# Performance work log

Measured on AMD Instinct MI355X. Metric: run time of the kernel, lower is better.

## Reference

```python
import jax, jax.numpy as jnp
import numpy as np

D = 1024
H = 16
DH = D // H

def setup_inputs() -> dict:
    key = jax.random.key(0)
    k1, k2, k3, k4 = jax.random.split(key, 4)
    x = jax.random.normal(k1, (4, 2048, D), dtype=jnp.float32)
    # qkv_linear: Linear(D, D, bias=False); weight stored as (out, in) torch-style
    w_qkv = jax.random.normal(k2, (D, D), dtype=jnp.float32) * (1.0 / np.sqrt(D))
    # final linear: Linear(D, D) with bias
    w_out = jax.random.normal(k3, (D, D), dtype=jnp.float32) * (1.0 / np.sqrt(D))
    b_out = jax.random.normal(k4, (D,), dtype=jnp.float32) * 0.01
    return {"x": x, "w_qkv": w_qkv, "w_out": w_out, "b_out": b_out}

def reference(x, w_qkv, w_out, b_out):
    B, S, E = x.shape
    # Same projection used for Q, K, V (faithful to original module)
    qkv = jnp.einsum('bse,de->bsd', x, w_qkv)           # [B,S,D]
    qkv = qkv.reshape(B, S, H, DH).transpose(0, 2, 1, 3)  # [B,H,S,Dh]
    q = k = v = qkv
    scale = DH ** -0.5
    attn = jnp.einsum('bhqd,bhkd->bhqk', q, k) * scale   # [B,H,S,S]
    attn = jax.nn.softmax(attn, axis=-1)
    out = jnp.einsum('bhqk,bhkd->bhqd', attn, v)         # [B,H,S,Dh]
    out = out.transpose(0, 2, 1, 3).reshape(B, S, E)
    return jnp.einsum('bse,de->bsd', out, w_out) + b_out
```

## Files before the change

kernel.cpp:

```cpp
#include <hip/hip_runtime.h>
#include <hip/hip_bf16.h>
#include <stdint.h>

typedef unsigned short u16;
typedef unsigned int   u32;
typedef unsigned long long u64;
typedef __bf16 bf16x8 __attribute__((ext_vector_type(8)));
typedef float  f32x4  __attribute__((ext_vector_type(4)));

#define D_MODEL 1024
#define NH 16
#define DHEAD 64
#define BB 4
#define SS 2048
#define MM (BB*SS)

__device__ __forceinline__ u16 f2bf(float f) {
    unsigned int u = __float_as_uint(f);
    u += 0x7fffu + ((u >> 16) & 1u);
    return (u16)(u >> 16);
}
__device__ __forceinline__ float bf2f(u16 s) {
    return __uint_as_float(((unsigned int)s) << 16);
}
__device__ __forceinline__ u32 pkbf(float a, float b) {
    __hip_bfloat162 h = __float22bfloat162_rn(make_float2(a, b));
    return *(u32*)&h;
}

union U8 {
    uint4 q;
    u16   v[8];
    bf16x8 f;
};

#define N4X (MM * D_MODEL / 4)
#define N4W (D_MODEL * D_MODEL / 4)
__global__ __launch_bounds__(256) void cvt_all_kernel(const float* __restrict__ x,
                                                      const float* __restrict__ wq,
                                                      const float* __restrict__ wo,
                                                      u16* __restrict__ xb,
                                                      u16* __restrict__ wqb,
                                                      u16* __restrict__ wob) {
    int i = blockIdx.x * 256 + threadIdx.x;
    const float* s; u16* d; int off;
    if (i < N4X)            { s = x;  d = xb;  off = i; }
    else if (i < N4X + N4W) { s = wq; d = wqb; off = i - N4X; }
    else                    { s = wo; d = wob; off = i - N4X - N4W; }
    float4 f = ((const float4*)s)[off];
    u32 o[2] = { pkbf(f.x, f.y), pkbf(f.z, f.w) };
    ((uint2*)d)[off] = *(const uint2*)o;
}

template <bool PERMUTE_OUT>
__device__ __forceinline__ void gemm_body(const u16* __restrict__ A,
                                          const u16* __restrict__ Bt,
                                          const float* __restrict__ Bo,
                                          u16* __restrict__ Cq, u16* __restrict__ CqT,
                                          float* __restrict__ Out)
{
    __shared__ __align__(16) u16 As[128*64];
    __shared__ __align__(16) u16 Bs[128*64];

    const int tid  = threadIdx.x;
    const int wave = tid >> 6;
    const int lane = tid & 63;
    const int quad = lane >> 4;
    const int l16  = lane & 15;
    const int bm = blockIdx.x >> 3;
    const int bn = blockIdx.x & 7;
    const int wm = wave >> 1, wn = wave & 1;

    f32x4 acc[4][4] = {};

    const int rp = tid >> 3;
    const int ch = tid & 7;
    const int sc = ch ^ (rp & 7);

    const u16* Ab = A  + (size_t)(bm * 128 + rp) * D_MODEL + sc * 8;
    const u16* Bb = Bt + (size_t)(bn * 128 + rp) * D_MODEL + sc * 8;
    const int xr = l16 & 7;

    for (int k0 = 0; k0 < D_MODEL; k0 += 64) {
#pragma unroll
        for (int p = 0; p < 4; ++p) {
            __builtin_amdgcn_global_load_lds(
                (__attribute__((address_space(1))) void*)(Ab + (size_t)(32*p) * D_MODEL + k0),
                (__attribute__((address_space(3))) void*)(As + p*2048 + tid*8), 16, 0, 0);
            __builtin_amdgcn_global_load_lds(
                (__attribute__((address_space(1))) void*)(Bb + (size_t)(32*p) * D_MODEL + k0),
                (__attribute__((address_space(3))) void*)(Bs + p*2048 + tid*8), 16, 0, 0);
        }
        __syncthreads();

#pragma unroll
        for (int ks = 0; ks < 2; ++ks) {
            bf16x8 af[4], bfr[4];
#pragma unroll
            for (int t = 0; t < 4; ++t)
                af[t] = *(const bf16x8*)(const void*)(
                    As + (wm*64 + t*16 + l16)*64 + (((ks*4 + quad) ^ xr) * 8));
#pragma unroll
            for (int t = 0; t < 4; ++t)
                bfr[t] = *(const bf16x8*)(const void*)(
                    Bs + (wn*64 + t*16 + l16)*64 + (((ks*4 + quad) ^ xr) * 8));
#pragma unroll
            for (int i = 0; i < 4; ++i)
#pragma unroll
                for (int j = 0; j < 4; ++j)
                    acc[i][j] = __builtin_amdgcn_mfma_f32_16x16x32_bf16(af[i], bfr[j], acc[i][j], 0, 0, 0);
        }
        __syncthreads();
    }

    const int rowbase = bm*128 + wm*64;
    const int colbase = bn*128 + wn*64;
    if (PERMUTE_OUT) {
#pragma unroll
        for (int j = 0; j < 4; ++j) {
            const int col = colbase + j*16 + l16;
            const int h = col >> 6, dh = col & 63;
#pragma unroll
            for (int i = 0; i < 4; ++i) {
                const int row0 = rowbase + i*16 + quad*4;
                const int b = row0 >> 11, s0 = row0 & (SS - 1);
#pragma unroll
                for (int r = 0; r < 4; ++r)
                    Cq[(((size_t)(b*NH + h))*SS + s0 + r)*DHEAD + dh] = f2bf(acc[i][j][r]);
                u64 w = (u64)pkbf(acc[i][j][0], acc[i][j][1])
                      | ((u64)pkbf(acc[i][j][2], acc[i][j][3]) << 32);
                *(u64*)(CqT + ((size_t)((b*NH + h)*DHEAD + dh))*SS + s0) = w;
            }
        }
    } else {
#pragma unroll
        for (int j = 0; j < 4; ++j) {
            const int col = colbase + j*16 + l16;
            const float bias = Bo[col];
#pragma unroll
            for (int i = 0; i < 4; ++i) {
#pragma unroll
                for (int r = 0; r < 4; ++r) {
                    const int row = rowbase + i*16 + quad*4 + r;
                    Out[(size_t)row * D_MODEL + col] = acc[i][j][r] + bias;
                }
            }
        }
    }
}

__global__ __launch_bounds__(256) void gemm_qkv_kernel(const u16* __restrict__ A,
                                                       const u16* __restrict__ Bt,
                                                       u16* __restrict__ Cq,
                                                       u16* __restrict__ CqT) {
    gemm_body<true>(A, Bt, nullptr, Cq, CqT, nullptr);
}

__global__ __launch_bounds__(256) void gemm_out_kernel(const u16* __restrict__ A,
                                                       const u16* __restrict__ Bt,
                                                       const float* __restrict__ Bo,
                                                       float* __restrict__ Out) {
    gemm_body<false>(A, Bt, Bo, nullptr, nullptr, Out);
}

__global__ __launch_bounds__(256, 4) void attn_kernel(const u16* __restrict__ qkv,
                                                      const u16* __restrict__ qkvT,
                                                      u16* __restrict__ outb)
{
    __shared__ __align__(16) u16 Ks[2*2048];
    __shared__ __align__(16) u16 Vt[2*2048];
    __shared__ __align__(16) u16 Pl[4*1280];

    const int tid  = threadIdx.x;
    const int wave = tid >> 6;
    const int lane = tid & 63;
    const int quad = lane >> 4;
    const int l16  = lane & 15;

    const int bh   = blockIdx.x >> 4;
    const int qblk = blockIdx.x & 15;
    const int b = bh >> 4, h = bh & 15;
    const int qbase = qblk * 128 + wave * 32;

    const u16* Qp = qkv + (size_t)bh * SS * DHEAD;
    const float qscale = 0.125f * 1.4426950408889634f;

    bf16x8 qb[2][2];
#pragma unroll
    for (int nt = 0; nt < 2; ++nt)
#pragma unroll
        for (int ks = 0; ks < 2; ++ks) {
            U8 raw; raw.q = *(const uint4*)(Qp + (size_t)(qbase + nt*16 + l16)*DHEAD + ks*32 + quad*8);
            U8 w;
#pragma unroll
            for (int jj = 0; jj < 4; ++jj)
                ((u32*)&w)[jj] = pkbf(bf2f(raw.v[2*jj]) * qscale, bf2f(raw.v[2*jj+1]) * qscale);
            qb[nt][ks] = w.f;
        }

    const int rK = tid >> 3, cK = (tid & 7) ^ ((rK >> 1) & 7);
    const u16* srcK = qkv  + (size_t)bh * SS * DHEAD + rK * DHEAD + cK * 8;
    const int rV = tid >> 2, cV = (tid & 3) ^ ((rV >> 1) & 3);
    const u16* srcV = qkvT + (size_t)bh * DHEAD * SS + (size_t)rV * SS + cV * 8;

    const int h8 = (l16 >> 1) & 7, h4 = (l16 >> 1) & 3;
    const int ko0 = l16*64 + ((quad)     ^ h8) * 8;
    const int ko1 = l16*64 + ((4 + quad) ^ h8) * 8;
    const int vo  = l16*32 + ((quad) ^ h4) * 8;

    u16* Pw       = Pl + wave*1280 + l16*40 + quad*4;
    const u16* Pr = Pl + wave*1280 + l16*40 + quad*8;

    bf16x8 ones;
#pragma unroll
    for (int j = 0; j < 8; ++j) ones[j] = (__bf16)1.0f;

    f32x4 ot[4][2] = {};
    f32x4 lsum[2]  = {};

    __builtin_amdgcn_global_load_lds(
        (__attribute__((address_space(1))) void*)(srcK),
        (__attribute__((address_space(3))) void*)(Ks + tid*8), 16, 0, 0);
    __builtin_amdgcn_global_load_lds(
        (__attribute__((address_space(1))) void*)(srcV),
        (__attribute__((address_space(3))) void*)(Vt + tid*8), 16, 0, 0);

#pragma unroll 2
    for (int kt = 0; kt < SS/32; ++kt) {
        __syncthreads();
        if (kt < SS/32 - 1) {
            __builtin_amdgcn_global_load_lds(
                (__attribute__((address_space(1))) void*)(srcK + (size_t)(kt+1)*32*DHEAD),
                (__attribute__((address_space(3))) void*)(Ks + ((kt+1)&1)*2048 + tid*8), 16, 0, 0);
            __builtin_amdgcn_global_load_lds(
                (__attribute__((address_space(1))) void*)(srcV + (kt+1)*32),
                (__attribute__((address_space(3))) void*)(Vt + ((kt+1)&1)*2048 + tid*8), 16, 0, 0);
        }
        const u16* Kb = Ks + (kt&1)*2048;
        const u16* Vb = Vt + (kt&1)*2048;

#pragma unroll
        for (int mt = 0; mt < 2; ++mt) {
            f32x4 s[2] = {};
            bf16x8 kf0 = *(const bf16x8*)(const void*)(Kb + mt*1024 + ko0);
            bf16x8 kf1 = *(const bf16x8*)(const void*)(Kb + mt*1024 + ko1);
#pragma unroll
            for (int nt = 0; nt < 2; ++nt)
                s[nt] = __builtin_amdgcn_mfma_f32_16x16x32_bf16(kf0, qb[nt][0], s[nt], 0, 0, 0);
#pragma unroll
            for (int nt = 0; nt < 2; ++nt)
                s[nt] = __builtin_amdgcn_mfma_f32_16x16x32_bf16(kf1, qb[nt][1], s[nt], 0, 0, 0);
#pragma unroll
            for (int nt = 0; nt < 2; ++nt) {
                float p0 = __builtin_amdgcn_exp2f(s[nt][0]);
                float p1 = __builtin_amdgcn_exp2f(s[nt][1]);
                float p2 = __builtin_amdgcn_exp2f(s[nt][2]);
                float p3 = __builtin_amdgcn_exp2f(s[nt][3]);
                u64 w = (u64)pkbf(p0, p1) | ((u64)pkbf(p2, p3) << 32);
                *(u64*)(Pw + nt*640 + mt*16) = w;
            }
        }

        bf16x8 pf[2];
#pragma unroll
        for (int nt = 0; nt < 2; ++nt)
            pf[nt] = *(const bf16x8*)(const void*)(Pr + nt*640);
#pragma unroll
        for (int nt = 0; nt < 2; ++nt)
            lsum[nt] = __builtin_amdgcn_mfma_f32_16x16x32_bf16(ones, pf[nt], lsum[nt], 0, 0, 0);
        bf16x8 vf[4];
#pragma unroll
        for (int dt = 0; dt < 4; ++dt)
            vf[dt] = *(const bf16x8*)(const void*)(Vb + dt*512 + vo);
#pragma unroll
        for (int dt = 0; dt < 4; ++dt)
#pragma unroll
            for (int nt = 0; nt < 2; ++nt)
                ot[dt][nt] = __builtin_amdgcn_mfma_f32_16x16x32_bf16(vf[dt], pf[nt], ot[dt][nt], 0, 0, 0);
    }

    float inv[2];
#pragma unroll
    for (int nt = 0; nt < 2; ++nt) inv[nt] = 1.0f / lsum[nt][0];
#pragma unroll
    for (int dt = 0; dt < 4; ++dt)
#pragma unroll
        for (int nt = 0; nt < 2; ++nt) {
            u64 w = (u64)pkbf(ot[dt][nt][0]*inv[nt], ot[dt][nt][1]*inv[nt])
                  | ((u64)pkbf(ot[dt][nt][2]*inv[nt], ot[dt][nt][3]*inv[nt]) << 32);
            *(u64*)(outb + ((size_t)(b*SS + qbase + nt*16 + l16))*D_MODEL
                         + h*64 + dt*16 + quad*4) = w;
        }
}

extern "C" void kernel_launch(void* const* d_in, const int* in_sizes, int n_in,
                              void* d_out, int out_size, void* d_ws, size_t ws_size,
                              hipStream_t stream)
{
    (void)in_sizes; (void)n_in; (void)out_size; (void)ws_size;
    const float* x  = (const float*)d_in[0];
    const float* wq = (const float*)d_in[1];
    const float* wo = (const float*)d_in[2];
    const float* bo = (const float*)d_in[3];

    char* ws = (char*)d_ws;
    u16* xb    = (u16*)(ws);
    u16* wqb   = (u16*)(ws + (size_t)(16 << 20));
    u16* wob   = (u16*)(ws + (size_t)(18 << 20));
    u16* qkvb  = (u16*)(ws + (size_t)(20 << 20));
    u16* qkvTb = (u16*)(ws + (size_t)(36 << 20));
    u16* attb  = xb;

    cvt_all_kernel<<<(N4X + 2*N4W) / 256, 256, 0, stream>>>(x, wq, wo, xb, wqb, wob);
    gemm_qkv_kernel<<<(MM/128) * (D_MODEL/128), 256, 0, stream>>>(xb, wqb, qkvb, qkvTb);
    attn_kernel<<<BB * NH * (SS/128), 256, 0, stream>>>(qkvb, qkvTb, attb);
    gemm_out_kernel<<<(MM/128) * (D_MODEL/128), 256, 0, stream>>>(attb, wob, bo, (float*)d_out);
}
```

Before: 236.5 us.

## Feed P directly from registers into 16x16x16 MFMA, drop LDS round-trip

The attention kernel no longer writes softmax probabilities P to shared memory and reads them back in a different layout. Instead the exp2 outputs stay in registers as s16x4 fragments and are consumed by 16x16x16 bf16 MFMAs, with V fragments loaded in a matching half-width layout. The row-sum uses scalar accumulation plus cross-lane shuffles instead of an extra MFMA against a ones vector, and s_setprio is raised around the MFMA blocks. This removes LDS traffic and shared memory use, at the cost of twice as many smaller MFMA instructions for the PV product. The row sum now adds the fp32 exponentials before bf16 rounding, so it is no longer computed from the same rounded values used in the PV product.

```diff
diff --git a/kernel.cpp b/kernel.cpp
--- a/kernel.cpp
+++ b/kernel.cpp
@@ -7,6 +7,7 @@
 typedef unsigned long long u64;
 typedef __bf16 bf16x8 __attribute__((ext_vector_type(8)));
 typedef float  f32x4  __attribute__((ext_vector_type(4)));
+typedef short  s16x4  __attribute__((ext_vector_type(4)));
 
 #define D_MODEL 1024
 #define NH 16
@@ -32,6 +33,10 @@
     uint4 q;
     u16   v[8];
     bf16x8 f;
+};
+union P4 {
+    u32   u[2];
+    s16x4 h;
 };
 
 #define N4X (MM * D_MODEL / 4)
@@ -169,7 +174,6 @@
 {
     __shared__ __align__(16) u16 Ks[2*2048];
     __shared__ __align__(16) u16 Vt[2*2048];
-    __shared__ __align__(16) u16 Pl[4*1280];
 
     const int tid  = threadIdx.x;
     const int wave = tid >> 6;
@@ -206,17 +210,11 @@
     const int h8 = (l16 >> 1) & 7, h4 = (l16 >> 1) & 3;
     const int ko0 = l16*64 + ((quad)     ^ h8) * 8;
     const int ko1 = l16*64 + ((4 + quad) ^ h8) * 8;
-    const int vo  = l16*32 + ((quad) ^ h4) * 8;
-
-    u16* Pw       = Pl + wave*1280 + l16*40 + quad*4;
-    const u16* Pr = Pl + wave*1280 + l16*40 + quad*8;
-
-    bf16x8 ones;
-#pragma unroll
-    for (int j = 0; j < 8; ++j) ones[j] = (__bf16)1.0f;
+    const int vo0 = l16*32 + (((quad >> 1))     ^ h4) * 8 + (quad & 1) * 4;
+    const int vo1 = l16*32 + ((2 + (quad >> 1)) ^ h4) * 8 + (quad & 1) * 4;
 
     f32x4 ot[4][2] = {};
-    f32x4 lsum[2]  = {};
+    float lacc[2]  = {0.0f, 0.0f};
 
     __builtin_amdgcn_global_load_lds(
         (__attribute__((address_space(1))) void*)(srcK),
@@ -239,49 +237,59 @@
         const u16* Kb = Ks + (kt&1)*2048;
         const u16* Vb = Vt + (kt&1)*2048;
 
+        s16x4 vfr[4][2];
+#pragma unroll
+        for (int dt = 0; dt < 4; ++dt) {
+            vfr[dt][0] = *(const s16x4*)(const void*)(Vb + dt*512 + vo0);
+            vfr[dt][1] = *(const s16x4*)(const void*)(Vb + dt*512 + vo1);
+        }
+
+        s16x4 pf[2][2];
 #pragma unroll
         for (int mt = 0; mt < 2; ++mt) {
             f32x4 s[2] = {};
             bf16x8 kf0 = *(const bf16x8*)(const void*)(Kb + mt*1024 + ko0);
             bf16x8 kf1 = *(const bf16x8*)(const void*)(Kb + mt*1024 + ko1);
+            __builtin_amdgcn_s_setprio(1);
 #pragma unroll
             for (int nt = 0; nt < 2; ++nt)
                 s[nt] = __builtin_amdgcn_mfma_f32_16x16x32_bf16(kf0, qb[nt][0], s[nt], 0, 0, 0);
 #pragma unroll
             for (int nt = 0; nt < 2; ++nt)
                 s[nt] = __builtin_amdgcn_mfma_f32_16x16x32_bf16(kf1, qb[nt][1], s[nt], 0, 0, 0);
+            __builtin_amdgcn_s_setprio(0);
 #pragma unroll
             for (int nt = 0; nt < 2; ++nt) {
                 float p0 = __builtin_amdgcn_exp2f(s[nt][0]);
                 float p1 = __builtin_amdgcn_exp2f(s[nt][1]);
                 float p2 = __builtin_amdgcn_exp2f(s[nt][2]);
                 float p3 = __builtin_amdgcn_exp2f(s[nt][3]);
-                u64 w = (u64)pkbf(p0, p1) | ((u64)pkbf(p2, p3) << 32);
-                *(u64*)(Pw + nt*640 + mt*16) = w;
+                lacc[nt] += (p0 + p1) + (p2 + p3);
+                P4 pk_; pk_.u[0] = pkbf(p0, p1); pk_.u[1] = pkbf(p2, p3);
+                pf[mt][nt] = pk_.h;
             }
         }
 
-        bf16x8 pf[2];
-#pragma unroll
-        for (int nt = 0; nt < 2; ++nt)
-            pf[nt] = *(const bf16x8*)(const void*)(Pr + nt*640);
-#pragma unroll
-        for (int nt = 0; nt < 2; ++nt)
-            lsum[nt] = __builtin_amdgcn_mfma_f32_16x16x32_bf16(ones, pf[nt], lsum[nt], 0, 0, 0);
-        bf16x8 vf[4];
+        __builtin_amdgcn_s_setprio(1);
 #pragma unroll
         for (int dt = 0; dt < 4; ++dt)
-            vf[dt] = *(const bf16x8*)(const void*)(Vb + dt*512 + vo);
-#pragma unroll
-        for (int dt = 0; dt < 4; ++dt)
-#pragma unroll
-            for (int nt = 0; nt < 2; ++nt)
-                ot[dt][nt] = __builtin_amdgcn_mfma_f32_16x16x32_bf16(vf[dt], pf[nt], ot[dt][nt], 0, 0, 0);
+#pragma unroll
+            for (int mt = 0; mt < 2; ++mt) {
+                ot[dt][0] = __builtin_amdgcn_mfma_f32_16x16x16bf16_1k(vfr[dt][mt], pf[mt][0], ot[dt][0], 0, 0, 0);
+                ot[dt][1] = __builtin_amdgcn_mfma_f32_16x16x16bf16_1k(vfr[dt][mt], pf[mt][1], ot[dt][1], 0, 0, 0);
+            }
+        __builtin_amdgcn_s_setprio(0);
     }
 
     float inv[2];
 #pragma unroll
-    for (int nt = 0; nt < 2; ++nt) inv[nt] = 1.0f / lsum[nt][0];
+    for (int nt = 0; nt < 2; ++nt) {
+        float v = lacc[nt];
+        v += __shfl_xor(v, 16, 64);
+        v += __shfl_xor(v, 32, 64);
+        inv[nt] = 1.0f / v;
+    }
+
 #pragma unroll
     for (int dt = 0; dt < 4; ++dt)
 #pragma unroll
```

New measurement: 239.6 us. Within noise of the previous version (+1.3%).
